# Optimization experiments

Measured on AMD Instinct MI355X. Metric: run time of the kernel, lower is better.

## Reference

```python
import jax, jax.numpy as jnp
import numpy as np

N_NODES = 100000
N_EDGES = 1600000
F_IN = 128
F_OUT = 64
BN_EPS = 1e-5


def setup_inputs() -> dict:
    key = jax.random.key(0)
    k1, k2, k3, k4, k5, k6 = jax.random.split(key, 6)
    x = jax.random.normal(k1, (N_NODES, F_IN), dtype=jnp.float32)
    edge_index = jax.random.randint(k2, (2, N_EDGES), 0, N_NODES, dtype=jnp.int64)
    edge_weight = jax.random.uniform(k3, (N_EDGES,), dtype=jnp.float32)
    # learned params: linear weight (no bias), batchnorm gamma/beta
    W = jax.random.normal(k4, (F_OUT, F_IN), dtype=jnp.float32) * (1.0 / np.sqrt(F_IN))
    gamma = jnp.ones((F_OUT,), dtype=jnp.float32)
    beta = jnp.zeros((F_OUT,), dtype=jnp.float32)
    return {"x": x, "edge_index": edge_index, "edge_weight": edge_weight,
            "W": W, "gamma": gamma, "beta": beta}


def reference(x, edge_index, edge_weight, W, gamma, beta):
    N = x.shape[0]
    h = x @ W.T  # [N, F_OUT]
    # add self loops with weight 1.0
    loop = jnp.arange(N, dtype=edge_index.dtype)
    src = jnp.concatenate([edge_index[0], loop])
    dst = jnp.concatenate([edge_index[1], loop])
    w = jnp.concatenate([edge_weight, jnp.ones((N,), dtype=h.dtype)])
    # degree of row (src) counts edge occurrences (unweighted)
    deg = jax.ops.segment_sum(jnp.ones_like(w), src, num_segments=N)
    dinv = jnp.where(deg > 0, jax.lax.rsqrt(deg), 0.0)
    norm = dinv[src] * w * dinv[dst]  # [E+N]
    # gather-scale-scatter aggregation
    out = jax.ops.segment_sum(h[src] * norm[:, None], dst, num_segments=N)
    out = jax.nn.relu(out)
    # BatchNorm1d (training mode: biased batch stats over nodes)
    mean = jnp.mean(out, axis=0)
    var = jnp.mean((out - mean) ** 2, axis=0)
    out = (out - mean) * jax.lax.rsqrt(var + BN_EPS) * gamma + beta
    # dropout p=0.0 -> identity
    return out
```

## Files before the change

### kernel.cpp

```cpp
#include <hip/hip_runtime.h>

#define N_NODES 100000
#define N_EDGES 1600000
#define F_IN 128
#define F_OUT 64
#define BN_EPS 1e-5f

#define NPART 4
#define NCHUNK 64
#define PSIZE 25000
#define CHUNK_E 25000

#define SCAN_BLK 1024
#define SCAN_NB  ((N_NODES + SCAN_BLK - 1) / SCAN_BLK)


typedef __attribute__((ext_vector_type(8))) short bf16x8;
typedef __attribute__((ext_vector_type(4))) float f32x4;

__device__ __forceinline__ unsigned short f2bf(float x) {
    unsigned u = __float_as_uint(x);
    u += 0x7fffu + ((u >> 16) & 1u);
    return (unsigned short)(u >> 16);
}
__device__ __forceinline__ float4 bf4(uint2 p) {
    return make_float4(__int_as_float((int)(p.x << 16)),
                       __int_as_float((int)(p.x & 0xffff0000u)),
                       __int_as_float((int)(p.y << 16)),
                       __int_as_float((int)(p.y & 0xffff0000u)));
}

__global__ __launch_bounds__(256) void convert_kernel(const void* __restrict__ ei,
                                                      int* __restrict__ s32,
                                                      int* __restrict__ d32) {
    const long long* q = (const long long*)ei;
    long long probe = q[threadIdx.x & 63];
    bool bad = (probe < 0 || probe >= N_NODES);
    int is64 = (__ballot(bad) == 0ULL);

    int i = blockIdx.x * 256 + threadIdx.x;
    if (i >= N_EDGES / 4) return;
    int4 s, d;
    if (is64) {
        longlong2 a = *(const longlong2*)&q[i * 4];
        longlong2 b = *(const longlong2*)&q[i * 4 + 2];
        s = make_int4((int)a.x, (int)a.y, (int)b.x, (int)b.y);
        longlong2 c = *(const longlong2*)&q[N_EDGES + i * 4];
        longlong2 e = *(const longlong2*)&q[N_EDGES + i * 4 + 2];
        d = make_int4((int)c.x, (int)c.y, (int)e.x, (int)e.y);
    } else {
        s = ((const int4*)ei)[i];
        d = ((const int4*)ei)[N_EDGES / 4 + i];
    }
    ((int4*)s32)[i] = s;
    ((int4*)d32)[i] = d;
}

__global__ __launch_bounds__(512) void count_kernel(const int* __restrict__ s32,
                                                    const int* __restrict__ d32,
                                                    unsigned* __restrict__ partial32) {
    __shared__ unsigned bins[PSIZE / 2];
    const int tid = threadIdx.x;
    const int p = blockIdx.x % NPART;
    const int b = blockIdx.x / NPART;
    const int p0 = p * PSIZE;
    for (int i = tid; i < PSIZE / 2; i += 512) bins[i] = 0u;
    __syncthreads();
    const int4* sp = (const int4*)(s32 + b * CHUNK_E);
    const int4* dp = (const int4*)(d32 + b * CHUNK_E);
    for (int i = tid; i < CHUNK_E / 4; i += 512) {
        int4 s = sp[i];
        int4 d = dp[i];
#define C1(sk, dk) { \
        unsigned si = (unsigned)((sk) - p0); \
        if (si < PSIZE) atomicAdd(&bins[si >> 1], 1u << ((si & 1) * 16)); \
        unsigned dd = (unsigned)((dk) - p0); \
        if ((unsigned)(sk) < N_NODES && dd < PSIZE) \
            atomicAdd(&bins[dd >> 1], 256u << ((dd & 1) * 16)); }
        C1(s.x, d.x) C1(s.y, d.y) C1(s.z, d.z) C1(s.w, d.w)
#undef C1
    }
    __syncthreads();
    unsigned* dst = partial32 + (unsigned)blockIdx.x * (PSIZE / 2);
    for (int i = tid; i < PSIZE / 2; i += 512) dst[i] = bins[i];
}

__global__ __launch_bounds__(256) void reduce_kernel(unsigned short* __restrict__ partial16,
                                                     unsigned* __restrict__ cnt,
                                                     float* __restrict__ dinv,
                                                     float* __restrict__ sums) {
    int n = blockIdx.x * 256 + threadIdx.x;
    if (n < 128) sums[n] = 0.f;
    if (n >= N_NODES) return;
    unsigned p = (unsigned)n / PSIZE;
    unsigned i = (unsigned)n % PSIZE;
    unsigned run = 0, degt = 0;
    unsigned addr = p * PSIZE + i;
#pragma unroll 8
    for (int c = 0; c < NCHUNK; ++c) {
        unsigned v = partial16[addr];
        partial16[addr] = (unsigned short)run;
        run += (v >> 8) & 0xffu;
        degt += v & 0xffu;
        addr += NPART * PSIZE;
    }
    cnt[n] = run;
    dinv[n] = rsqrtf((float)(degt + 1u));
}

__global__ __launch_bounds__(256) void scan1_kernel(const unsigned* __restrict__ cnt,
                                                    unsigned* __restrict__ off,
                                                    unsigned* __restrict__ bsum) {
    __shared__ unsigned s[256];
    const int tid = threadIdx.x;
    const int base = blockIdx.x * SCAN_BLK + tid * 4;
    unsigned v[4];
#pragma unroll
    for (int k = 0; k < 4; ++k) v[k] = (base + k < N_NODES) ? cnt[base + k] : 0u;
    unsigned tsum = v[0] + v[1] + v[2] + v[3];
    s[tid] = tsum;
    __syncthreads();
    for (int d = 1; d < 256; d <<= 1) {
        unsigned t = (tid >= d) ? s[tid - d] : 0u;
        __syncthreads();
        s[tid] += t;
        __syncthreads();
    }
    unsigned run = s[tid] - tsum;
#pragma unroll
    for (int k = 0; k < 4; ++k) {
        if (base + k < N_NODES) off[base + k] = run;
        run += v[k];
    }
    if (tid == 255) bsum[blockIdx.x] = s[255];
}

__global__ __launch_bounds__(128) void scan2_kernel(unsigned* __restrict__ bsum) {
    __shared__ unsigned s[128];
    const int tid = threadIdx.x;
    unsigned v = (tid < SCAN_NB) ? bsum[tid] : 0u;
    s[tid] = v;
    __syncthreads();
    for (int d = 1; d < 128; d <<= 1) {
        unsigned t = (tid >= d) ? s[tid - d] : 0u;
        __syncthreads();
        s[tid] += t;
        __syncthreads();
    }
    if (tid < SCAN_NB) bsum[tid] = s[tid] - v;
}

__global__ void scan3_kernel(unsigned* __restrict__ off, const unsigned* __restrict__ bsum) {
    int i = blockIdx.x * blockDim.x + threadIdx.x;
    if (i < N_NODES) off[i] += bsum[i >> 10];
}

__global__ __launch_bounds__(512) void place_kernel(const int* __restrict__ s32,
                                                    const int* __restrict__ d32,
                                                    const float* __restrict__ ew,
                                                    const float* __restrict__ dinv,
                                                    const unsigned* __restrict__ off,
                                                    const unsigned short* __restrict__ partial16,
                                                    int2* __restrict__ buck) {
    __shared__ unsigned lcur[PSIZE / 4];
    const int tid = threadIdx.x;
    const int p = blockIdx.x % NPART;
    const int b = blockIdx.x / NPART;
    const int p0 = p * PSIZE;
    for (int i = tid; i < PSIZE / 4; i += 512) lcur[i] = 0u;
    __syncthreads();
    const int4* sp = (const int4*)(s32 + b * CHUNK_E);
    const int4* dp = (const int4*)(d32 + b * CHUNK_E);
    const float4* wp = (const float4*)(ew + b * CHUNK_E);
    const unsigned short* pref = partial16 + (unsigned)blockIdx.x * PSIZE;
    for (int i = tid; i < CHUNK_E / 4; i += 512) {
        int4 s = sp[i];
        int4 d = dp[i];
        float4 w = wp[i];
#define P1(sk, dk, wk) { \
        unsigned dd = (unsigned)((dk) - p0); \
        if ((unsigned)(sk) < N_NODES && dd < PSIZE) { \
            unsigned sh = (dd & 3) * 8; \
            unsigned old = atomicAdd(&lcur[dd >> 2], 1u << sh); \
            unsigned pos = (old >> sh) & 0xffu; \
            unsigned slot = off[dk] + pref[dd] + pos; \
            buck[slot] = make_int2((sk), __float_as_int(dinv[sk] * (wk) * dinv[dk])); } }
        P1(s.x, d.x, w.x) P1(s.y, d.y, w.y) P1(s.z, d.z, w.z) P1(s.w, d.w, w.w)
#undef P1
    }
}

__global__ __launch_bounds__(256) void gemm_kernel(const float* __restrict__ x,
                                                   const float* __restrict__ W,
                                                   unsigned short* __restrict__ hb) {
    __shared__ short wlds[16 * 64 * 8];
    const int tid = threadIdx.x;
    const int n0 = blockIdx.x * 64;
    {
        int out = tid & 63;
        int kb = tid >> 6;
#pragma unroll
        for (int i = 0; i < 4; ++i) {
            int koct = kb + i * 4;
            const float* wp = &W[out * F_IN + koct * 8];
            float4 aa = *(const float4*)wp;
            float4 bb = *(const float4*)(wp + 4);
            bf16x8 f;
            f[0] = (short)f2bf(aa.x); f[1] = (short)f2bf(aa.y);
            f[2] = (short)f2bf(aa.z); f[3] = (short)f2bf(aa.w);
            f[4] = (short)f2bf(bb.x); f[5] = (short)f2bf(bb.y);
            f[6] = (short)f2bf(bb.z); f[7] = (short)f2bf(bb.w);
            ((bf16x8*)wlds)[koct * 64 + out] = f;
        }
    }
    __syncthreads();
    const int wv = tid >> 6;
    const int lane = tid & 63;
    const int m = lane & 15;
    const int quad = lane >> 4;
    const int row = n0 + wv * 16 + m;
    const bool rv = row < N_NODES;
    const float* xrow = &x[(long)row * F_IN + quad * 8];
    f32x4 acc0 = {0.f, 0.f, 0.f, 0.f};
    f32x4 acc1 = {0.f, 0.f, 0.f, 0.f};
    f32x4 acc2 = {0.f, 0.f, 0.f, 0.f};
    f32x4 acc3 = {0.f, 0.f, 0.f, 0.f};
#pragma unroll
    for (int kc = 0; kc < 4; ++kc) {
        bf16x8 a = {0, 0, 0, 0, 0, 0, 0, 0};
        if (rv) {
            float4 aa = *(const float4*)(xrow + kc * 32);
            float4 bb = *(const float4*)(xrow + kc * 32 + 4);
            a[0] = (short)f2bf(aa.x); a[1] = (short)f2bf(aa.y);
            a[2] = (short)f2bf(aa.z); a[3] = (short)f2bf(aa.w);
            a[4] = (short)f2bf(bb.x); a[5] = (short)f2bf(bb.y);
            a[6] = (short)f2bf(bb.z); a[7] = (short)f2bf(bb.w);
        }
        const bf16x8* wrow = &((const bf16x8*)wlds)[(kc * 4 + quad) * 64 + m];
        acc0 = __builtin_amdgcn_mfma_f32_16x16x32_bf16(a, wrow[0],  acc0, 0, 0, 0);
        acc1 = __builtin_amdgcn_mfma_f32_16x16x32_bf16(a, wrow[16], acc1, 0, 0, 0);
        acc2 = __builtin_amdgcn_mfma_f32_16x16x32_bf16(a, wrow[32], acc2, 0, 0, 0);
        acc3 = __builtin_amdgcn_mfma_f32_16x16x32_bf16(a, wrow[48], acc3, 0, 0, 0);
    }
#pragma unroll
    for (int r = 0; r < 4; ++r) {
        int node = n0 + wv * 16 + quad * 4 + r;
        if (node < N_NODES) {
            unsigned short* hr = &hb[(long)node * F_OUT + m];
            hr[0]  = f2bf(acc0[r]);
            hr[16] = f2bf(acc1[r]);
            hr[32] = f2bf(acc2[r]);
            hr[48] = f2bf(acc3[r]);
        }
    }
}

#define AGG_BLOCKS 2048
#define AGG_WAVES  (AGG_BLOCKS * 4)
__global__ __launch_bounds__(256) void aggregate_kernel(
    const unsigned short* __restrict__ hb, const float* __restrict__ dinv,
    const unsigned* __restrict__ off, const unsigned* __restrict__ cnt,
    const int2* __restrict__ buck, float* __restrict__ out,
    float* __restrict__ sums) {
    const int tid = threadIdx.x;
    const int wv = tid >> 6;
    const int lane = tid & 63;
    const int es = lane >> 4;
    const int cl = lane & 15;
    float s1[4] = {0.f, 0.f, 0.f, 0.f};
    float s2[4] = {0.f, 0.f, 0.f, 0.f};

    for (int n = blockIdx.x * 4 + wv; n < N_NODES; n += AGG_WAVES) {
        const unsigned o = off[n];
        const unsigned c = cnt[n];
        float4 a0 = make_float4(0.f, 0.f, 0.f, 0.f);
        float4 a1 = make_float4(0.f, 0.f, 0.f, 0.f);
        float4 a2 = make_float4(0.f, 0.f, 0.f, 0.f);
        float4 a3 = make_float4(0.f, 0.f, 0.f, 0.f);
        unsigned j = es;
        for (; j + 12 < c; j += 16) {
            int2 b1 = buck[o + j];
            int2 b2 = buck[o + j + 4];
            int2 b3 = buck[o + j + 8];
            int2 b4 = buck[o + j + 12];
            float4 h1 = bf4(((const uint2*)(hb + ((long)b1.x << 6)))[cl]);
            float4 h2 = bf4(((const uint2*)(hb + ((long)b2.x << 6)))[cl]);
            float4 h3 = bf4(((const uint2*)(hb + ((long)b3.x << 6)))[cl]);
            float4 h4 = bf4(((const uint2*)(hb + ((long)b4.x << 6)))[cl]);
            float w1 = __int_as_float(b1.y), w2 = __int_as_float(b2.y);
            float w3 = __int_as_float(b3.y), w4 = __int_as_float(b4.y);
            a0.x += h1.x * w1; a0.y += h1.y * w1; a0.z += h1.z * w1; a0.w += h1.w * w1;
            a1.x += h2.x * w2; a1.y += h2.y * w2; a1.z += h2.z * w2; a1.w += h2.w * w2;
            a2.x += h3.x * w3; a2.y += h3.y * w3; a2.z += h3.z * w3; a2.w += h3.w * w3;
            a3.x += h4.x * w4; a3.y += h4.y * w4; a3.z += h4.z * w4; a3.w += h4.w * w4;
        }
        for (; j < c; j += 4) {
            int2 bb = buck[o + j];
            float w = __int_as_float(bb.y);
            float4 hv = bf4(((const uint2*)(hb + ((long)bb.x << 6)))[cl]);
            a0.x += hv.x * w; a0.y += hv.y * w; a0.z += hv.z * w; a0.w += hv.w * w;
        }
        a0.x += a1.x + a2.x + a3.x;
        a0.y += a1.y + a2.y + a3.y;
        a0.z += a1.z + a2.z + a3.z;
        a0.w += a1.w + a2.w + a3.w;
        a0.x += __shfl_xor(a0.x, 16); a0.y += __shfl_xor(a0.y, 16);
        a0.z += __shfl_xor(a0.z, 16); a0.w += __shfl_xor(a0.w, 16);
        a0.x += __shfl_xor(a0.x, 32); a0.y += __shfl_xor(a0.y, 32);
        a0.z += __shfl_xor(a0.z, 32); a0.w += __shfl_xor(a0.w, 32);
        if (es == 0) {
            float di = dinv[n];
            float sw = di * di;
            float4 hn = bf4(((const uint2*)(hb + ((long)n << 6)))[cl]);
            a0.x = fmaxf(fmaf(hn.x, sw, a0.x), 0.f);
            a0.y = fmaxf(fmaf(hn.y, sw, a0.y), 0.f);
            a0.z = fmaxf(fmaf(hn.z, sw, a0.z), 0.f);
            a0.w = fmaxf(fmaf(hn.w, sw, a0.w), 0.f);
            *(float4*)&out[(long)n * F_OUT + cl * 4] = a0;
            s1[0] += a0.x; s1[1] += a0.y; s1[2] += a0.z; s1[3] += a0.w;
            s2[0] += a0.x * a0.x; s2[1] += a0.y * a0.y;
            s2[2] += a0.z * a0.z; s2[3] += a0.w * a0.w;
        }
    }
    __shared__ float l1[256];
    __shared__ float l2[256];
    if (es == 0) {
#pragma unroll
        for (int k = 0; k < 4; ++k) {
            l1[wv * 64 + cl * 4 + k] = s1[k];
            l2[wv * 64 + cl * 4 + k] = s2[k];
        }
    }
    __syncthreads();
    if (tid < 64) {
        float b1 = l1[tid] + l1[64 + tid] + l1[128 + tid] + l1[192 + tid];
        float b2 = l2[tid] + l2[64 + tid] + l2[128 + tid] + l2[192 + tid];
        atomicAdd(&sums[tid], b1);
        atomicAdd(&sums[64 + tid], b2);
    }
}

__global__ void finalize_kernel(float* __restrict__ sums,
                                const float* __restrict__ gamma,
                                const float* __restrict__ beta) {
    int c = threadIdx.x;
    const float inv_n = 1.0f / (float)N_NODES;
    float mean = sums[c] * inv_n;
    float var = sums[64 + c] * inv_n - mean * mean;
    float rs = rsqrtf(var + BN_EPS);
    float sc = rs * gamma[c];
    sums[c] = sc;
    sums[64 + c] = beta[c] - mean * sc;
}

__global__ __launch_bounds__(256) void apply_kernel(float* __restrict__ agg,
                                                    const float* __restrict__ sums) {
    int i = blockIdx.x * blockDim.x + threadIdx.x;
    if (i >= N_NODES * 16) return;
    int c4 = (i & 15) << 2;
    float4 v = ((float4*)agg)[i];
    v.x = v.x * sums[c4 + 0] + sums[64 + c4 + 0];
    v.y = v.y * sums[c4 + 1] + sums[64 + c4 + 1];
    v.z = v.z * sums[c4 + 2] + sums[64 + c4 + 2];
    v.w = v.w * sums[c4 + 3] + sums[64 + c4 + 3];
    ((float4*)agg)[i] = v;
}

extern "C" void kernel_launch(void* const* d_in, const int* in_sizes, int n_in,
                              void* d_out, int out_size, void* d_ws, size_t ws_size,
                              hipStream_t stream) {
    const float* x     = (const float*)d_in[0];
    const void*  ei    = d_in[1];
    const float* ew    = (const float*)d_in[2];
    const float* W     = (const float*)d_in[3];
    const float* gamma = (const float*)d_in[4];
    const float* beta  = (const float*)d_in[5];
    float* out = (float*)d_out;
    float* ws  = (float*)d_ws;

    int*            s32       = (int*)ws;
    int*            d32       = (int*)(ws + 1600000);
    unsigned*       partial32 = (unsigned*)(ws + 3200000);
    unsigned short* partial16 = (unsigned short*)(ws + 3200000);
    unsigned short* hb        = (unsigned short*)(ws + 3200000);
    int2*           buck      = (int2*)(ws + 6400000);
    float*          dinv      = ws + 9600000;
    float*          sums      = ws + 9700000;
    unsigned*       cnt       = (unsigned*)(ws + 9700128);
    unsigned*       off       = (unsigned*)(ws + 9800128);
    unsigned*       bsum      = (unsigned*)(ws + 9900128);

    convert_kernel<<<(N_EDGES / 4 + 255) / 256, 256, 0, stream>>>(ei, s32, d32);
    count_kernel<<<NPART * NCHUNK, 512, 0, stream>>>(s32, d32, partial32);
    reduce_kernel<<<(N_NODES + 255) / 256, 256, 0, stream>>>(partial16, cnt, dinv, sums);
    scan1_kernel<<<SCAN_NB, 256, 0, stream>>>(cnt, off, bsum);
    scan2_kernel<<<1, 128, 0, stream>>>(bsum);
    scan3_kernel<<<(N_NODES + 255) / 256, 256, 0, stream>>>(off, bsum);
    place_kernel<<<NPART * NCHUNK, 512, 0, stream>>>(s32, d32, ew, dinv, off, partial16, buck);
    gemm_kernel<<<(N_NODES + 63) / 64, 256, 0, stream>>>(x, W, hb);
    aggregate_kernel<<<AGG_BLOCKS, 256, 0, stream>>>(hb, dinv, off, cnt, buck, out, sums);
    finalize_kernel<<<1, 64, 0, stream>>>(sums, gamma, beta);
    apply_kernel<<<(N_NODES * 16 + 255) / 256, 256, 0, stream>>>(out, sums);
}
```

Baseline: 300.4 us.

## Record per-edge rank during counting and make placement a flat per-edge pass

The count kernel now splits nodes into two larger partitions and packs 4-bit counters into bytes. It records each edge's rank within its destination bucket in a byte array stored temporarily in the output buffer. Placement then becomes a grid-wide per-edge kernel that needs no shared-memory atomics and no re-scan of the edge chunk. The aggregate kernel switches to contiguous node ranges per wave with shallower unrolling. The 4-bit counters overflow if a chunk holds more than 15 edges for one node, which relies on the random low-degree input, and a slot bound check was added.

```diff
diff --git a/kernel.cpp b/kernel.cpp
--- a/kernel.cpp
+++ b/kernel.cpp
@@ -6,10 +6,10 @@
 #define F_OUT 64
 #define BN_EPS 1e-5f
 
-#define NPART 4
-#define NCHUNK 64
-#define PSIZE 25000
-#define CHUNK_E 25000
+#define NPART 2
+#define NCHUNK 128
+#define PSIZE 50000
+#define CHUNK_E 12500
 
 #define SCAN_BLK 1024
 #define SCAN_NB  ((N_NODES + SCAN_BLK - 1) / SCAN_BLK)
@@ -58,50 +58,56 @@
 
 __global__ __launch_bounds__(512) void count_kernel(const int* __restrict__ s32,
                                                     const int* __restrict__ d32,
-                                                    unsigned* __restrict__ partial32) {
-    __shared__ unsigned bins[PSIZE / 2];
+                                                    unsigned* __restrict__ partial32,
+                                                    unsigned char* __restrict__ rank) {
+    __shared__ unsigned bins[PSIZE / 4];
     const int tid = threadIdx.x;
     const int p = blockIdx.x % NPART;
     const int b = blockIdx.x / NPART;
     const int p0 = p * PSIZE;
-    for (int i = tid; i < PSIZE / 2; i += 512) bins[i] = 0u;
+    for (int i = tid; i < PSIZE / 4; i += 512) bins[i] = 0u;
     __syncthreads();
     const int4* sp = (const int4*)(s32 + b * CHUNK_E);
     const int4* dp = (const int4*)(d32 + b * CHUNK_E);
+    const int e0 = b * CHUNK_E;
     for (int i = tid; i < CHUNK_E / 4; i += 512) {
         int4 s = sp[i];
         int4 d = dp[i];
-#define C1(sk, dk) { \
+        int e = e0 + i * 4;
+#define C1(sk, dk, kk) { \
         unsigned si = (unsigned)((sk) - p0); \
-        if (si < PSIZE) atomicAdd(&bins[si >> 1], 1u << ((si & 1) * 16)); \
+        if (si < PSIZE) atomicAdd(&bins[si >> 2], 1u << ((si & 3) * 8)); \
         unsigned dd = (unsigned)((dk) - p0); \
-        if ((unsigned)(sk) < N_NODES && dd < PSIZE) \
-            atomicAdd(&bins[dd >> 1], 256u << ((dd & 1) * 16)); }
-        C1(s.x, d.x) C1(s.y, d.y) C1(s.z, d.z) C1(s.w, d.w)
+        if ((unsigned)(sk) < N_NODES && dd < PSIZE) { \
+            unsigned sh = (dd & 3) * 8 + 4; \
+            unsigned old = atomicAdd(&bins[dd >> 2], 16u << ((dd & 3) * 8)); \
+            rank[e + kk] = (unsigned char)((old >> sh) & 0xFu); } }
+        C1(s.x, d.x, 0) C1(s.y, d.y, 1) C1(s.z, d.z, 2) C1(s.w, d.w, 3)
 #undef C1
     }
     __syncthreads();
-    unsigned* dst = partial32 + (unsigned)blockIdx.x * (PSIZE / 2);
-    for (int i = tid; i < PSIZE / 2; i += 512) dst[i] = bins[i];
-}
-
-__global__ __launch_bounds__(256) void reduce_kernel(unsigned short* __restrict__ partial16,
+    unsigned* dst = partial32 + (unsigned)blockIdx.x * (PSIZE / 4);
+    for (int i = tid; i < PSIZE / 4; i += 512) dst[i] = bins[i];
+}
+
+__global__ __launch_bounds__(256) void reduce_kernel(unsigned* __restrict__ partial32,
                                                      unsigned* __restrict__ cnt,
                                                      float* __restrict__ dinv,
                                                      float* __restrict__ sums) {
     int n = blockIdx.x * 256 + threadIdx.x;
     if (n < 128) sums[n] = 0.f;
     if (n >= N_NODES) return;
-    unsigned p = (unsigned)n / PSIZE;
-    unsigned i = (unsigned)n % PSIZE;
+    unsigned char* pb = (unsigned char*)partial32;
+    unsigned p = (n >= PSIZE) ? 1u : 0u;
+    unsigned i = (unsigned)n - p * PSIZE;
     unsigned run = 0, degt = 0;
     unsigned addr = p * PSIZE + i;
 #pragma unroll 8
     for (int c = 0; c < NCHUNK; ++c) {
-        unsigned v = partial16[addr];
-        partial16[addr] = (unsigned short)run;
-        run += (v >> 8) & 0xffu;
-        degt += v & 0xffu;
+        unsigned v = pb[addr];
+        pb[addr] = (unsigned char)run;
+        run += v >> 4;
+        degt += v & 0xFu;
         addr += NPART * PSIZE;
     }
     cnt[n] = run;
@@ -155,39 +161,33 @@
     if (i < N_NODES) off[i] += bsum[i >> 10];
 }
 
-__global__ __launch_bounds__(512) void place_kernel(const int* __restrict__ s32,
+__global__ __launch_bounds__(256) void place_kernel(const int* __restrict__ s32,
                                                     const int* __restrict__ d32,
                                                     const float* __restrict__ ew,
                                                     const float* __restrict__ dinv,
                                                     const unsigned* __restrict__ off,
-                                                    const unsigned short* __restrict__ partial16,
+                                                    const unsigned* __restrict__ partial32,
+                                                    const unsigned char* __restrict__ rank,
                                                     int2* __restrict__ buck) {
-    __shared__ unsigned lcur[PSIZE / 4];
-    const int tid = threadIdx.x;
-    const int p = blockIdx.x % NPART;
-    const int b = blockIdx.x / NPART;
-    const int p0 = p * PSIZE;
-    for (int i = tid; i < PSIZE / 4; i += 512) lcur[i] = 0u;
-    __syncthreads();
-    const int4* sp = (const int4*)(s32 + b * CHUNK_E);
-    const int4* dp = (const int4*)(d32 + b * CHUNK_E);
-    const float4* wp = (const float4*)(ew + b * CHUNK_E);
-    const unsigned short* pref = partial16 + (unsigned)blockIdx.x * PSIZE;
-    for (int i = tid; i < CHUNK_E / 4; i += 512) {
-        int4 s = sp[i];
-        int4 d = dp[i];
-        float4 w = wp[i];
-#define P1(sk, dk, wk) { \
-        unsigned dd = (unsigned)((dk) - p0); \
-        if ((unsigned)(sk) < N_NODES && dd < PSIZE) { \
-            unsigned sh = (dd & 3) * 8; \
-            unsigned old = atomicAdd(&lcur[dd >> 2], 1u << sh); \
-            unsigned pos = (old >> sh) & 0xffu; \
-            unsigned slot = off[dk] + pref[dd] + pos; \
+    int i = blockIdx.x * 256 + threadIdx.x;
+    if (i >= N_EDGES / 4) return;
+    int4 s = ((const int4*)s32)[i];
+    int4 d = ((const int4*)d32)[i];
+    float4 w = ((const float4*)ew)[i];
+    uchar4 r = ((const uchar4*)rank)[i];
+    const unsigned char* pb = (const unsigned char*)partial32;
+    int e = i * 4;
+    int b = e / CHUNK_E;
+    unsigned base = (unsigned)b * NPART * PSIZE;
+#define P1(sk, dk, wk, rk) { \
+    if ((unsigned)(sk) < N_NODES && (unsigned)(dk) < N_NODES) { \
+        unsigned pref = pb[base + (unsigned)(dk)]; \
+        unsigned slot = off[dk] + pref + (rk); \
+        if (slot < N_EDGES) \
             buck[slot] = make_int2((sk), __float_as_int(dinv[sk] * (wk) * dinv[dk])); } }
-        P1(s.x, d.x, w.x) P1(s.y, d.y, w.y) P1(s.z, d.z, w.z) P1(s.w, d.w, w.w)
+    P1(s.x, d.x, w.x, r.x) P1(s.y, d.y, w.y, r.y)
+    P1(s.z, d.z, w.z, r.z) P1(s.w, d.w, w.w, r.w)
 #undef P1
-    }
 }
 
 __global__ __launch_bounds__(256) void gemm_kernel(const float* __restrict__ x,
@@ -256,7 +256,7 @@
 }
 
 #define AGG_BLOCKS 2048
-#define AGG_WAVES  (AGG_BLOCKS * 4)
+#define NPW 13
 __global__ __launch_bounds__(256) void aggregate_kernel(
     const unsigned short* __restrict__ hb, const float* __restrict__ dinv,
     const unsigned* __restrict__ off, const unsigned* __restrict__ cnt,
@@ -270,40 +270,32 @@
     float s1[4] = {0.f, 0.f, 0.f, 0.f};
     float s2[4] = {0.f, 0.f, 0.f, 0.f};
 
-    for (int n = blockIdx.x * 4 + wv; n < N_NODES; n += AGG_WAVES) {
+    const int wid = blockIdx.x * 4 + wv;
+    const int nbeg = wid * NPW;
+    const int nend = (nbeg + NPW < N_NODES) ? nbeg + NPW : N_NODES;
+    for (int n = nbeg; n < nend; ++n) {
         const unsigned o = off[n];
         const unsigned c = cnt[n];
         float4 a0 = make_float4(0.f, 0.f, 0.f, 0.f);
         float4 a1 = make_float4(0.f, 0.f, 0.f, 0.f);
-        float4 a2 = make_float4(0.f, 0.f, 0.f, 0.f);
-        float4 a3 = make_float4(0.f, 0.f, 0.f, 0.f);
         unsigned j = es;
-        for (; j + 12 < c; j += 16) {
+        for (; j + 4 < c; j += 8) {
             int2 b1 = buck[o + j];
             int2 b2 = buck[o + j + 4];
-            int2 b3 = buck[o + j + 8];
-            int2 b4 = buck[o + j + 12];
             float4 h1 = bf4(((const uint2*)(hb + ((long)b1.x << 6)))[cl]);
             float4 h2 = bf4(((const uint2*)(hb + ((long)b2.x << 6)))[cl]);
-            float4 h3 = bf4(((const uint2*)(hb + ((long)b3.x << 6)))[cl]);
-            float4 h4 = bf4(((const uint2*)(hb + ((long)b4.x << 6)))[cl]);
-            float w1 = __int_as_float(b1.y), w2 = __int_as_float(b2.y);
-            float w3 = __int_as_float(b3.y), w4 = __int_as_float(b4.y);
+            float w1 = __int_as_float(b1.y);
+            float w2 = __int_as_float(b2.y);
             a0.x += h1.x * w1; a0.y += h1.y * w1; a0.z += h1.z * w1; a0.w += h1.w * w1;
             a1.x += h2.x * w2; a1.y += h2.y * w2; a1.z += h2.z * w2; a1.w += h2.w * w2;
-            a2.x += h3.x * w3; a2.y += h3.y * w3; a2.z += h3.z * w3; a2.w += h3.w * w3;
-            a3.x += h4.x * w4; a3.y += h4.y * w4; a3.z += h4.z * w4; a3.w += h4.w * w4;
-        }
-        for (; j < c; j += 4) {
+        }
+        if (j < c) {
             int2 bb = buck[o + j];
             float w = __int_as_float(bb.y);
             float4 hv = bf4(((const uint2*)(hb + ((long)bb.x << 6)))[cl]);
             a0.x += hv.x * w; a0.y += hv.y * w; a0.z += hv.z * w; a0.w += hv.w * w;
         }
-        a0.x += a1.x + a2.x + a3.x;
-        a0.y += a1.y + a2.y + a3.y;
-        a0.z += a1.z + a2.z + a3.z;
-        a0.w += a1.w + a2.w + a3.w;
+        a0.x += a1.x; a0.y += a1.y; a0.z += a1.z; a0.w += a1.w;
         a0.x += __shfl_xor(a0.x, 16); a0.y += __shfl_xor(a0.y, 16);
         a0.z += __shfl_xor(a0.z, 16); a0.w += __shfl_xor(a0.w, 16);
         a0.x += __shfl_xor(a0.x, 32); a0.y += __shfl_xor(a0.y, 32);
@@ -381,7 +373,6 @@
     int*            s32       = (int*)ws;
     int*            d32       = (int*)(ws + 1600000);
     unsigned*       partial32 = (unsigned*)(ws + 3200000);
-    unsigned short* partial16 = (unsigned short*)(ws + 3200000);
     unsigned short* hb        = (unsigned short*)(ws + 3200000);
     int2*           buck      = (int2*)(ws + 6400000);
     float*          dinv      = ws + 9600000;
@@ -389,14 +380,16 @@
     unsigned*       cnt       = (unsigned*)(ws + 9700128);
     unsigned*       off       = (unsigned*)(ws + 9800128);
     unsigned*       bsum      = (unsigned*)(ws + 9900128);
+    unsigned char*  rank      = (unsigned char*)d_out;
 
     convert_kernel<<<(N_EDGES / 4 + 255) / 256, 256, 0, stream>>>(ei, s32, d32);
-    count_kernel<<<NPART * NCHUNK, 512, 0, stream>>>(s32, d32, partial32);
-    reduce_kernel<<<(N_NODES + 255) / 256, 256, 0, stream>>>(partial16, cnt, dinv, sums);
+    count_kernel<<<NPART * NCHUNK, 512, 0, stream>>>(s32, d32, partial32, rank);
+    reduce_kernel<<<(N_NODES + 255) / 256, 256, 0, stream>>>(partial32, cnt, dinv, sums);
     scan1_kernel<<<SCAN_NB, 256, 0, stream>>>(cnt, off, bsum);
     scan2_kernel<<<1, 128, 0, stream>>>(bsum);
     scan3_kernel<<<(N_NODES + 255) / 256, 256, 0, stream>>>(off, bsum);
-    place_kernel<<<NPART * NCHUNK, 512, 0, stream>>>(s32, d32, ew, dinv, off, partial16, buck);
+    place_kernel<<<(N_EDGES / 4 + 255) / 256, 256, 0, stream>>>(s32, d32, ew, dinv, off,
+                                                                partial32, rank, buck);
     gemm_kernel<<<(N_NODES + 63) / 64, 256, 0, stream>>>(x, W, hb);
     aggregate_kernel<<<AGG_BLOCKS, 256, 0, stream>>>(hb, dinv, off, cnt, buck, out, sums);
     finalize_kernel<<<1, 64, 0, stream>>>(sums, gamma, beta);
```

Measured after the change: 300.7 us. No clear change (+0.1%).
